# Optimization experiments

Hardware: AMD Instinct MI355X
Metric: run time of the kernel (lower is better)

The kernel has to match this reference:

```python
import jax, jax.numpy as jnp
import numpy as np

LN_EPS = 1e-5


def layer_norm(x, gamma, beta):
    mu = jnp.mean(x, axis=-1, keepdims=True)
    var = jnp.mean(jnp.square(x - mu), axis=-1, keepdims=True)
    return (x - mu) * jax.lax.rsqrt(var + LN_EPS) * gamma + beta


def setup_inputs() -> dict:
    key = jax.random.key(0)
    ks = jax.random.split(key, 7)
    B, S, D = 8, 1024, 512
    H, Dh = 8, 64
    scale = 1.0 / np.sqrt(D)
    x = jax.random.normal(ks[0], (B, S, D), dtype=jnp.float32)
    Wq = jax.random.normal(ks[1], (D, H * Dh), dtype=jnp.float32) * scale
    Wk = jax.random.normal(ks[2], (D, H * Dh), dtype=jnp.float32) * scale
    Wv = jax.random.normal(ks[3], (D, H * Dh), dtype=jnp.float32) * scale
    Wfc = jax.random.normal(ks[4], (H * Dh, D), dtype=jnp.float32) * scale
    gamma = jnp.ones((D,), dtype=jnp.float32)
    beta = jnp.zeros((D,), dtype=jnp.float32)
    return {"x": x, "Wq": Wq, "Wk": Wk, "Wv": Wv, "Wfc": Wfc, "gamma": gamma, "beta": beta}


def reference(x, Wq, Wk, Wv, Wfc, gamma, beta):
    B, S, D = x.shape
    H, Dh = 8, 64
    Q = (x @ Wq).reshape(B, S, H, Dh).transpose(0, 2, 1, 3)  # [B,H,S,Dh]
    K = (x @ Wk).reshape(B, S, H, Dh).transpose(0, 2, 1, 3)
    V = (x @ Wv).reshape(B, S, H, Dh).transpose(0, 2, 1, 3)
    scores = jnp.einsum('bhqd,bhkd->bhqk', Q, K) / np.sqrt(Dh).astype(np.float32)
    # tridiagonal band mask; NOTE: original fills off-band with -1e-09 (not -inf)
    idx = jnp.arange(S)
    band = jnp.abs(idx[:, None] - idx[None, :]) <= 1  # [S,S]
    scores = jnp.where(band, scores, jnp.float32(-1e-09))
    attn = jax.nn.softmax(scores, axis=-1)
    context = jnp.einsum('bhqk,bhkd->bhqd', attn, V)  # [B,H,S,Dh]
    context = context.transpose(0, 2, 1, 3).reshape(B, S, H * Dh)
    out = context @ Wfc
    return layer_norm(out + x, gamma, beta)
```

## Files before the change

kernel.cpp:

```cpp
#include <hip/hip_runtime.h>
#include <math.h>


typedef short     s8v  __attribute__((ext_vector_type(8)));
typedef float     f4v  __attribute__((ext_vector_type(4)));
typedef unsigned short us4v __attribute__((ext_vector_type(4)));
typedef unsigned short us8v __attribute__((ext_vector_type(8)));

__device__ __forceinline__ unsigned short f2b(float f) {
  union { float f; unsigned int u; } v; v.f = f;
  unsigned int u = v.u;
  return (unsigned short)((u + 0x7fffu + ((u >> 16) & 1u)) >> 16);
}
__device__ __forceinline__ float b2f(unsigned short u) {
  union { unsigned int i; float f; } v; v.i = ((unsigned int)u) << 16;
  return v.f;
}
__device__ __forceinline__ void gload_lds16(const void* g, void* l) {
  __builtin_amdgcn_global_load_lds(
      (const __attribute__((address_space(1))) void*)g,
      (__attribute__((address_space(3))) void*)l, 16, 0, 0);
}

__global__ __launch_bounds__(256) void conv_kernel(
    const float* __restrict__ x,
    const float* __restrict__ Wq, const float* __restrict__ Wk,
    const float* __restrict__ Wv, const float* __restrict__ Wfc,
    unsigned short* __restrict__ xb, unsigned short* __restrict__ Wt,
    float* __restrict__ Vsum) {
  __shared__ unsigned short tile[32][33];
  const int bid = blockIdx.x, t = threadIdx.x;
  if (bid < 4096) {
    const int i = bid * 256 + t;
    const float4 f = ((const float4*)x)[i];
    us4v o; o[0] = f2b(f.x); o[1] = f2b(f.y); o[2] = f2b(f.z); o[3] = f2b(f.w);
    ((us4v*)xb)[i] = o;
  } else if (bid < 5120) {
    const int id = bid - 4096;
    const int z = id >> 8, rem = id & 255;
    const int bx = rem & 15, by = rem >> 4;
    const float* W = (z == 0) ? Wq : (z == 1) ? Wk : (z == 2) ? Wv : Wfc;
    const int tx = t & 31, ty = t >> 5;
    const int n0 = bx * 32, k0 = by * 32;
    #pragma unroll
    for (int r = ty; r < 32; r += 8)
      tile[r][tx] = f2b(W[(size_t)(k0 + r) * 512 + n0 + tx]);
    __syncthreads();
    unsigned short* dst = Wt + (size_t)z * 512 * 512;
    #pragma unroll
    for (int r = ty; r < 32; r += 8)
      dst[(size_t)(n0 + r) * 512 + k0 + tx] = tile[tx][r];
  } else {
    float4 zz = {0.f, 0.f, 0.f, 0.f};
    #pragma unroll
    for (int p = 0; p < 4; ++p) ((float4*)Vsum)[p * 256 + t] = zz;
  }
}

__global__ __launch_bounds__(512, 2) void gemm_qkv_kernel(
    const unsigned short* __restrict__ A, const unsigned short* __restrict__ Bt,
    unsigned short* __restrict__ C, float* __restrict__ Vsum) {
  const int N = 1536, K = 512;
  __shared__ __align__(16) unsigned short smem[65536];
  const int t = threadIdx.x, wave = t >> 6, lane = t & 63;
  const int wrr = wave >> 2, wcc = wave & 3;
  const int quad = lane >> 4, l16 = lane & 15;
  const int bm = blockIdx.y * 128, bn = blockIdx.x * 384;

  const unsigned short* gA[2];
  #pragma unroll
  for (int p = 0; p < 2; ++p) {
    const int ci = wave * 128 + p * 64 + lane;
    const int r = ci >> 3, c = (ci & 7) ^ (r & 7);
    gA[p] = A + (size_t)(bm + r) * K + c * 8;
  }
  const unsigned short* gB[6];
  #pragma unroll
  for (int p = 0; p < 6; ++p) {
    const int ci = wave * 384 + p * 64 + lane;
    const int r = ci >> 3, c = (ci & 7) ^ (r & 7);
    gB[p] = Bt + (size_t)(bn + r) * K + c * 8;
  }

  f4v acc[4][6];
  #pragma unroll
  for (int i = 0; i < 4; ++i)
    #pragma unroll
    for (int j = 0; j < 6; ++j) {
      f4v z = {0.f, 0.f, 0.f, 0.f};
      acc[i][j] = z;
    }

  #pragma unroll
  for (int p = 0; p < 2; ++p)
    gload_lds16(gA[p], smem + (wave * 128 + p * 64) * 8);
  #pragma unroll
  for (int p = 0; p < 6; ++p)
    gload_lds16(gB[p], smem + 8192 + (wave * 384 + p * 64) * 8);
  __syncthreads();

  #pragma unroll
  for (int it = 0; it < 8; ++it) {
    const int cur = (it & 1) * 32768;
    const int nxt = 32768 - cur;
    const unsigned short* Ab = smem + cur;
    const unsigned short* Bb = smem + cur + 8192;

    s8v af0[4], af1[4];
    #pragma unroll
    for (int i = 0; i < 4; ++i) {
      const int r = wrr * 64 + i * 16 + l16;
      af0[i] = *(const s8v*)&Ab[(r * 8 + (quad ^ (r & 7))) * 8];
      af1[i] = *(const s8v*)&Ab[(r * 8 + ((quad + 4) ^ (r & 7))) * 8];
    }
    s8v bf0[6];
    #pragma unroll
    for (int j = 0; j < 6; ++j) {
      const int n = wcc * 96 + j * 16 + l16;
      bf0[j] = *(const s8v*)&Bb[(n * 8 + (quad ^ (n & 7))) * 8];
    }
    if (it < 7) {
      const int kt = (it + 1) * 64;
      #pragma unroll
      for (int p = 0; p < 2; ++p)
        gload_lds16(gA[p] + kt, smem + nxt + (wave * 128 + p * 64) * 8);
      #pragma unroll
      for (int p = 0; p < 6; ++p)
        gload_lds16(gB[p] + kt, smem + nxt + 8192 + (wave * 384 + p * 64) * 8);
    }
    #pragma unroll
    for (int i = 0; i < 4; ++i)
      #pragma unroll
      for (int j = 0; j < 6; ++j)
        acc[i][j] = __builtin_amdgcn_mfma_f32_16x16x32_bf16(
            af0[i], bf0[j], acc[i][j], 0, 0, 0);
    #pragma unroll
    for (int j = 0; j < 6; ++j) {
      const int n = wcc * 96 + j * 16 + l16;
      const s8v bf1 = *(const s8v*)&Bb[(n * 8 + ((quad + 4) ^ (n & 7))) * 8];
      #pragma unroll
      for (int i = 0; i < 4; ++i)
        acc[i][j] = __builtin_amdgcn_mfma_f32_16x16x32_bf16(
            af1[i], bf1, acc[i][j], 0, 0, 0);
    }
    __syncthreads();
  }

  {
    const int b = bm >> 10;
    #pragma unroll
    for (int j = 0; j < 6; ++j) {
      const int gc = bn + wcc * 96 + j * 16 + l16;
      float ps = 0.f;
      #pragma unroll
      for (int i = 0; i < 4; ++i)
        #pragma unroll
        for (int r = 0; r < 4; ++r) ps += acc[i][j][r];
      ps += __shfl_xor(ps, 16);
      ps += __shfl_xor(ps, 32);
      if (quad == 0 && gc >= 1024)
        atomicAdd(&Vsum[b * 512 + gc - 1024], ps);
    }
  }

  #pragma unroll
  for (int i = 0; i < 4; ++i) {
    const int lr0 = wrr * 64 + i * 16 + quad * 4;
    #pragma unroll
    for (int j = 0; j < 6; ++j) {
      const int lc = wcc * 96 + j * 16 + l16;
      #pragma unroll
      for (int r = 0; r < 4; ++r)
        smem[(lr0 + r) * 392 + lc] = f2b(acc[i][j][r]);
    }
  }
  __syncthreads();
  #pragma unroll
  for (int p = 0; p < 12; ++p) {
    const int row = t >> 2;
    const int ch  = p * 4 + (t & 3);
    *(us8v*)(C + (size_t)(bm + row) * N + bn + ch * 8) =
        *(const us8v*)&smem[row * 392 + ch * 8];
  }
}

__device__ __forceinline__ void attn_load(
    const unsigned short* __restrict__ QKV, const float* __restrict__ Vsum,
    size_t oq, size_t om, size_t op, int vsbase, int co,
    us4v& qv, us4v& km, us4v& k0, us4v& kp,
    us4v& vm, us4v& v0, us4v& vp, float4& vs) {
  qv = *(const us4v*)(QKV + oq + co);
  km = *(const us4v*)(QKV + om + 512 + co);
  k0 = *(const us4v*)(QKV + oq + 512 + co);
  kp = *(const us4v*)(QKV + op + 512 + co);
  vm = *(const us4v*)(QKV + om + 1024 + co);
  v0 = *(const us4v*)(QKV + oq + 1024 + co);
  vp = *(const us4v*)(QKV + op + 1024 + co);
  vs = *(const float4*)(Vsum + vsbase + co);
}

__device__ __forceinline__ void attn_compute(
    int qq, int arow, int al, int h, unsigned short* ctxS,
    us4v qv, us4v km, us4v k0, us4v kp,
    us4v vm, us4v v0, us4v vp, float4 vs) {
  float pm = 0.f, p0 = 0.f, pp = 0.f;
  #pragma unroll
  for (int r = 0; r < 4; ++r) {
    const float qf = b2f(qv[r]);
    pm += qf * b2f(km[r]);
    p0 += qf * b2f(k0[r]);
    pp += qf * b2f(kp[r]);
  }
  #pragma unroll
  for (int m = 1; m < 16; m <<= 1) {
    pm += __shfl_xor(pm, m);
    p0 += __shfl_xor(p0, m);
    pp += __shfl_xor(pp, m);
  }
  const float OFF = -1e-9f;
  const float s0 = p0 * 0.125f;
  const float sm = (qq > 0)    ? pm * 0.125f : OFF;
  const float sp = (qq < 1023) ? pp * 0.125f : OFF;
  const float mx = fmaxf(fmaxf(s0, sm), fmaxf(sp, OFF));
  const float e0 = __expf(s0 - mx), em = __expf(sm - mx), ep = __expf(sp - mx);
  const float eoff = __expf(OFF - mx);
  const float inv  = 1.f / (e0 + em + ep + 1021.f * eoff);
  const float wm = (em - eoff) * inv, w0 = (e0 - eoff) * inv,
              wp = (ep - eoff) * inv, wt = eoff * inv;
  us4v o;
  const float* vsf = (const float*)&vs;
  #pragma unroll
  for (int r = 0; r < 4; ++r)
    o[r] = f2b(wt * vsf[r] + wm * b2f(vm[r]) + w0 * b2f(v0[r]) +
               wp * b2f(vp[r]));
  const int ch   = h * 8 + (al >> 1);
  const int slot = (ch & 56) | ((ch & 7) ^ (arow & 7));
  *(us4v*)&ctxS[arow * 512 + slot * 8 + (al & 1) * 4] = o;
}

#define OS 516

__global__ __launch_bounds__(512) void attn_fcln_kernel(
    const unsigned short* __restrict__ QKV,
    const float* __restrict__ Vsum,
    const unsigned short* __restrict__ Bt,
    const unsigned short* __restrict__ xb, const float* __restrict__ gamma,
    const float* __restrict__ beta, float* __restrict__ y) {
  const int K = 512;
  __shared__ __align__(16) unsigned short smem[81920];
  unsigned short* ctxS = smem + 65536;
  float* outS = (float*)smem;

  const int t = threadIdx.x, wave = t >> 6, lane = t & 63;
  const int bm = blockIdx.x * 32;

  const unsigned short* gB[8];
  #pragma unroll
  for (int p = 0; p < 8; ++p) {
    const int ci = wave * 512 + p * 64 + lane;
    const int r = ci >> 3, c = (ci & 7) ^ (r & 7);
    gB[p] = Bt + (size_t)r * K + c * 8;
  }

  const int arow = t >> 4, al = t & 15;
  const int b = bm >> 10;
  const int qq = (bm & 1023) + arow;
  const int qm = qq > 0 ? qq - 1 : 0;
  const int qp = qq < 1023 ? qq + 1 : 1023;
  const size_t rowb = (size_t)b * 1024 * 1536;
  const size_t oq = rowb + (size_t)qq * 1536;
  const size_t om = rowb + (size_t)qm * 1536;
  const size_t op = rowb + (size_t)qp * 1536;
  const int vsbase = b * 512;

  {
    us4v qv, km, k0, kp, vm, v0, vp; float4 vs;
    attn_load(QKV, Vsum, oq, om, op, vsbase, al * 4,
              qv, km, k0, kp, vm, v0, vp, vs);
    #pragma unroll
    for (int p = 0; p < 8; ++p)
      gload_lds16(gB[p], smem + wave * 4096 + p * 512);
    attn_compute(qq, arow, al, 0, ctxS, qv, km, k0, kp, vm, v0, vp, vs);
  }
  __syncthreads();

  const int wrr = wave >> 2, wcc = wave & 3;
  const int quad = lane >> 4, l16 = lane & 15;

  f4v acc[8];
  #pragma unroll
  for (int j = 0; j < 8; ++j) {
    f4v z = {0.f, 0.f, 0.f, 0.f};
    acc[j] = z;
  }

  #pragma unroll
  for (int it = 0; it < 8; ++it) {
    const int cur = (it & 1) * 32768;
    const int nxt = 32768 - cur;
    const unsigned short* Bb = smem + cur;

    us4v qv, km, k0, kp, vm, v0, vp; float4 vs;
    if (it < 7)
      attn_load(QKV, Vsum, oq, om, op, vsbase, (it + 1) * 64 + al * 4,
                qv, km, k0, kp, vm, v0, vp, vs);

    const int rm = wrr * 16 + l16;
    const s8v af0 =
        *(const s8v*)&ctxS[rm * 512 + (it * 8 + (quad ^ (rm & 7))) * 8];
    const s8v af1 =
        *(const s8v*)&ctxS[rm * 512 + (it * 8 + ((quad + 4) ^ (rm & 7))) * 8];
    s8v bf0[8];
    #pragma unroll
    for (int j = 0; j < 8; ++j) {
      const int n = wcc * 128 + j * 16 + l16;
      bf0[j] = *(const s8v*)&Bb[(n * 8 + (quad ^ (n & 7))) * 8];
    }
    if (it < 7) {
      const int kt = (it + 1) * 64;
      #pragma unroll
      for (int p = 0; p < 8; ++p)
        gload_lds16(gB[p] + kt, smem + nxt + wave * 4096 + p * 512);
    }
    #pragma unroll
    for (int j = 0; j < 8; ++j)
      acc[j] = __builtin_amdgcn_mfma_f32_16x16x32_bf16(af0, bf0[j], acc[j], 0, 0, 0);
    #pragma unroll
    for (int j = 0; j < 8; ++j) {
      const int n = wcc * 128 + j * 16 + l16;
      const s8v bf1 = *(const s8v*)&Bb[(n * 8 + ((quad + 4) ^ (n & 7))) * 8];
      acc[j] = __builtin_amdgcn_mfma_f32_16x16x32_bf16(af1, bf1, acc[j], 0, 0, 0);
    }
    if (it < 7)
      attn_compute(qq, arow, al, it + 1, ctxS, qv, km, k0, kp, vm, v0, vp, vs);
    __syncthreads();
  }

  #pragma unroll
  for (int j = 0; j < 8; ++j) {
    const int col = wcc * 128 + j * 16 + l16;
    const int row0 = wrr * 16 + quad * 4;
    #pragma unroll
    for (int r = 0; r < 4; ++r)
      outS[(row0 + r) * OS + col] = acc[j][r];
  }
  __syncthreads();

  const int row = t >> 4, l = t & 15;
  const size_t gbase = (size_t)(bm + row) * 512;
  float4 v[8];
  float s1 = 0.f, s2 = 0.f;
  #pragma unroll
  for (int k = 0; k < 8; ++k) {
    const int c = k * 64 + l * 4;
    const float4 a = *(const float4*)&outS[row * OS + c];
    const us4v xv = *(const us4v*)&xb[gbase + c];
    float4 w;
    w.x = a.x + b2f(xv[0]); w.y = a.y + b2f(xv[1]);
    w.z = a.z + b2f(xv[2]); w.w = a.w + b2f(xv[3]);
    v[k] = w;
    s1 += w.x + w.y + w.z + w.w;
    s2 += w.x * w.x + w.y * w.y + w.z * w.z + w.w * w.w;
  }
  #pragma unroll
  for (int m = 1; m < 16; m <<= 1) {
    s1 += __shfl_xor(s1, m);
    s2 += __shfl_xor(s2, m);
  }
  const float mu  = s1 * (1.f / 512.f);
  const float var = s2 * (1.f / 512.f) - mu * mu;
  const float rs  = rsqrtf(var + 1e-5f);
  #pragma unroll
  for (int k = 0; k < 8; ++k) {
    const int c = k * 64 + l * 4;
    const float4 g  = *(const float4*)&gamma[c];
    const float4 bb = *(const float4*)&beta[c];
    float4 o;
    o.x = (v[k].x - mu) * rs * g.x + bb.x;
    o.y = (v[k].y - mu) * rs * g.y + bb.y;
    o.z = (v[k].z - mu) * rs * g.z + bb.z;
    o.w = (v[k].w - mu) * rs * g.w + bb.w;
    *(float4*)&y[gbase + c] = o;
  }
}

extern "C" void kernel_launch(void* const* d_in, const int* in_sizes, int n_in,
                              void* d_out, int out_size, void* d_ws, size_t ws_size,
                              hipStream_t stream) {
  const float* x     = (const float*)d_in[0];
  const float* Wq    = (const float*)d_in[1];
  const float* Wk    = (const float*)d_in[2];
  const float* Wv    = (const float*)d_in[3];
  const float* Wfc   = (const float*)d_in[4];
  const float* gamma = (const float*)d_in[5];
  const float* beta  = (const float*)d_in[6];
  float* y = (float*)d_out;

  char* ws = (char*)d_ws;
  unsigned short* Wt   = (unsigned short*)(ws);
  unsigned short* xb   = (unsigned short*)(ws + 2097152);
  unsigned short* QKV  = (unsigned short*)(ws + 10485760);
  float*          Vsum = (float*)(ws + 35651584);

  conv_kernel<<<5121, 256, 0, stream>>>(x, Wq, Wk, Wv, Wfc, xb, Wt, Vsum);
  gemm_qkv_kernel<<<dim3(4, 64), 512, 0, stream>>>(xb, Wt, QKV, Vsum);
  attn_fcln_kernel<<<256, 512, 0, stream>>>(
      QKV, Vsum, Wt + (size_t)1536 * 512, xb, gamma, beta, y);
}
```

Before: 117.3 us.

## Fuse x bf16 conversion into QKV GEMM A-tile loads, read fp32 x in LN

Drops the separate pass that converted x to bf16. The QKV GEMM now loads fp32 x directly, converts it in registers and writes it to LDS in software-pipelined fashion, while still using async global-to-LDS loads for the weights. The residual add in the final layernorm now reads fp32 x instead of the bf16 copy. This removes a full read and write of x plus a bf16 readback, at the cost of more VGPR pressure and VALU work inside the GEMM loop. A side effect is better residual precision.

```diff
diff --git a/kernel.cpp b/kernel.cpp
--- a/kernel.cpp
+++ b/kernel.cpp
@@ -23,21 +23,13 @@
 }
 
 __global__ __launch_bounds__(256) void conv_kernel(
-    const float* __restrict__ x,
     const float* __restrict__ Wq, const float* __restrict__ Wk,
     const float* __restrict__ Wv, const float* __restrict__ Wfc,
-    unsigned short* __restrict__ xb, unsigned short* __restrict__ Wt,
-    float* __restrict__ Vsum) {
+    unsigned short* __restrict__ Wt, float* __restrict__ Vsum) {
   __shared__ unsigned short tile[32][33];
   const int bid = blockIdx.x, t = threadIdx.x;
-  if (bid < 4096) {
-    const int i = bid * 256 + t;
-    const float4 f = ((const float4*)x)[i];
-    us4v o; o[0] = f2b(f.x); o[1] = f2b(f.y); o[2] = f2b(f.z); o[3] = f2b(f.w);
-    ((us4v*)xb)[i] = o;
-  } else if (bid < 5120) {
-    const int id = bid - 4096;
-    const int z = id >> 8, rem = id & 255;
+  if (bid < 1024) {
+    const int z = bid >> 8, rem = bid & 255;
     const int bx = rem & 15, by = rem >> 4;
     const float* W = (z == 0) ? Wq : (z == 1) ? Wk : (z == 2) ? Wv : Wfc;
     const int tx = t & 31, ty = t >> 5;
@@ -58,7 +50,7 @@
 }
 
 __global__ __launch_bounds__(512, 2) void gemm_qkv_kernel(
-    const unsigned short* __restrict__ A, const unsigned short* __restrict__ Bt,
+    const float* __restrict__ x, const unsigned short* __restrict__ Bt,
     unsigned short* __restrict__ C, float* __restrict__ Vsum) {
   const int N = 1536, K = 512;
   __shared__ __align__(16) unsigned short smem[65536];
@@ -67,13 +59,12 @@
   const int quad = lane >> 4, l16 = lane & 15;
   const int bm = blockIdx.y * 128, bn = blockIdx.x * 384;
 
-  const unsigned short* gA[2];
-  #pragma unroll
-  for (int p = 0; p < 2; ++p) {
-    const int ci = wave * 128 + p * 64 + lane;
-    const int r = ci >> 3, c = (ci & 7) ^ (r & 7);
-    gA[p] = A + (size_t)(bm + r) * K + c * 8;
-  }
+  const int ciA0 = t, ciA1 = t + 512;
+  const int rA0 = ciA0 >> 3, cA0 = (ciA0 & 7) ^ (rA0 & 7);
+  const int rA1 = ciA1 >> 3, cA1 = (ciA1 & 7) ^ (rA1 & 7);
+  const float* gxA0 = x + (size_t)(bm + rA0) * K + cA0 * 8;
+  const float* gxA1 = x + (size_t)(bm + rA1) * K + cA1 * 8;
+
   const unsigned short* gB[6];
   #pragma unroll
   for (int p = 0; p < 6; ++p) {
@@ -91,12 +82,22 @@
       acc[i][j] = z;
     }
 
-  #pragma unroll
-  for (int p = 0; p < 2; ++p)
-    gload_lds16(gA[p], smem + (wave * 128 + p * 64) * 8);
-  #pragma unroll
-  for (int p = 0; p < 6; ++p)
-    gload_lds16(gB[p], smem + 8192 + (wave * 384 + p * 64) * 8);
+  {
+    const float4 a00 = *(const float4*)(gxA0);
+    const float4 a01 = *(const float4*)(gxA0 + 4);
+    const float4 a10 = *(const float4*)(gxA1);
+    const float4 a11 = *(const float4*)(gxA1 + 4);
+    #pragma unroll
+    for (int p = 0; p < 6; ++p)
+      gload_lds16(gB[p], smem + 8192 + (wave * 384 + p * 64) * 8);
+    us8v w0, w1;
+    w0[0] = f2b(a00.x); w0[1] = f2b(a00.y); w0[2] = f2b(a00.z); w0[3] = f2b(a00.w);
+    w0[4] = f2b(a01.x); w0[5] = f2b(a01.y); w0[6] = f2b(a01.z); w0[7] = f2b(a01.w);
+    w1[0] = f2b(a10.x); w1[1] = f2b(a10.y); w1[2] = f2b(a10.z); w1[3] = f2b(a10.w);
+    w1[4] = f2b(a11.x); w1[5] = f2b(a11.y); w1[6] = f2b(a11.z); w1[7] = f2b(a11.w);
+    *(us8v*)&smem[ciA0 * 8] = w0;
+    *(us8v*)&smem[ciA1 * 8] = w1;
+  }
   __syncthreads();
 
   #pragma unroll
@@ -105,6 +106,15 @@
     const int nxt = 32768 - cur;
     const unsigned short* Ab = smem + cur;
     const unsigned short* Bb = smem + cur + 8192;
+    const int kt = (it + 1) * 64;
+
+    float4 a00, a01, a10, a11;
+    if (it < 7) {
+      a00 = *(const float4*)(gxA0 + kt);
+      a01 = *(const float4*)(gxA0 + kt + 4);
+      a10 = *(const float4*)(gxA1 + kt);
+      a11 = *(const float4*)(gxA1 + kt + 4);
+    }
 
     s8v af0[4], af1[4];
     #pragma unroll
@@ -120,10 +130,6 @@
       bf0[j] = *(const s8v*)&Bb[(n * 8 + (quad ^ (n & 7))) * 8];
     }
     if (it < 7) {
-      const int kt = (it + 1) * 64;
-      #pragma unroll
-      for (int p = 0; p < 2; ++p)
-        gload_lds16(gA[p] + kt, smem + nxt + (wave * 128 + p * 64) * 8);
       #pragma unroll
       for (int p = 0; p < 6; ++p)
         gload_lds16(gB[p] + kt, smem + nxt + 8192 + (wave * 384 + p * 64) * 8);
@@ -134,6 +140,15 @@
       for (int j = 0; j < 6; ++j)
         acc[i][j] = __builtin_amdgcn_mfma_f32_16x16x32_bf16(
             af0[i], bf0[j], acc[i][j], 0, 0, 0);
+    if (it < 7) {
+      us8v w0, w1;
+      w0[0] = f2b(a00.x); w0[1] = f2b(a00.y); w0[2] = f2b(a00.z); w0[3] = f2b(a00.w);
+      w0[4] = f2b(a01.x); w0[5] = f2b(a01.y); w0[6] = f2b(a01.z); w0[7] = f2b(a01.w);
+      w1[0] = f2b(a10.x); w1[1] = f2b(a10.y); w1[2] = f2b(a10.z); w1[3] = f2b(a10.w);
+      w1[4] = f2b(a11.x); w1[5] = f2b(a11.y); w1[6] = f2b(a11.z); w1[7] = f2b(a11.w);
+      *(us8v*)&smem[nxt + ciA0 * 8] = w0;
+      *(us8v*)&smem[nxt + ciA1 * 8] = w1;
+    }
     #pragma unroll
     for (int j = 0; j < 6; ++j) {
       const int n = wcc * 96 + j * 16 + l16;
@@ -244,7 +259,7 @@
     const unsigned short* __restrict__ QKV,
     const float* __restrict__ Vsum,
     const unsigned short* __restrict__ Bt,
-    const unsigned short* __restrict__ xb, const float* __restrict__ gamma,
+    const float* __restrict__ x, const float* __restrict__ gamma,
     const float* __restrict__ beta, float* __restrict__ y) {
   const int K = 512;
   __shared__ __align__(16) unsigned short smem[81920];
@@ -353,11 +368,11 @@
   #pragma unroll
   for (int k = 0; k < 8; ++k) {
     const int c = k * 64 + l * 4;
-    const float4 a = *(const float4*)&outS[row * OS + c];
-    const us4v xv = *(const us4v*)&xb[gbase + c];
+    const float4 a  = *(const float4*)&outS[row * OS + c];
+    const float4 xa = *(const float4*)&x[gbase + c];
     float4 w;
-    w.x = a.x + b2f(xv[0]); w.y = a.y + b2f(xv[1]);
-    w.z = a.z + b2f(xv[2]); w.w = a.w + b2f(xv[3]);
+    w.x = a.x + xa.x; w.y = a.y + xa.y;
+    w.z = a.z + xa.z; w.w = a.w + xa.w;
     v[k] = w;
     s1 += w.x + w.y + w.z + w.w;
     s2 += w.x * w.x + w.y * w.y + w.z * w.z + w.w * w.w;
@@ -398,12 +413,11 @@
 
   char* ws = (char*)d_ws;
   unsigned short* Wt   = (unsigned short*)(ws);
-  unsigned short* xb   = (unsigned short*)(ws + 2097152);
   unsigned short* QKV  = (unsigned short*)(ws + 10485760);
   float*          Vsum = (float*)(ws + 35651584);
 
-  conv_kernel<<<5121, 256, 0, stream>>>(x, Wq, Wk, Wv, Wfc, xb, Wt, Vsum);
-  gemm_qkv_kernel<<<dim3(4, 64), 512, 0, stream>>>(xb, Wt, QKV, Vsum);
+  conv_kernel<<<1025, 256, 0, stream>>>(Wq, Wk, Wv, Wfc, Wt, Vsum);
+  gemm_qkv_kernel<<<dim3(4, 64), 512, 0, stream>>>(x, Wt, QKV, Vsum);
   attn_fcln_kernel<<<256, 512, 0, stream>>>(
-      QKV, Vsum, Wt + (size_t)1536 * 512, xb, gamma, beta, y);
-}
+      QKV, Vsum, Wt + (size_t)1536 * 512, x, gamma, beta, y);
+}
```

Result: slower. 123.8 us (+5.5%).
